# Performance work log

Hardware: AMD Instinct MI355X
Metric: run time of the kernel (lower is better)

Reference implementation:

```python
import jax, jax.numpy as jnp
import numpy as np

# Config (scaled-down DeepSeek-style MoE)
B, S, H = 4, 1024, 1024       # batch, seq, hidden_size
I = 512                        # intermediate_size per expert
E = 64                         # num_routed_experts
K = 8                          # top-k
C = 1024
NS = 1                         # num_shared_experts


def setup_inputs() -> dict:
    key = jax.random.key(0)
    ks = jax.random.split(key, 8)
    def w(k, shape, fan_in):
        return jax.random.normal(k, shape, jnp.float32) / np.float32(np.sqrt(fan_in))
    return {
        "hidden_states": jax.random.normal(ks[0], (B, S, H), jnp.float32),
        "gate_w":    w(ks[1], (E, H), H),            # nn.Linear(H, E).weight
        "shared_wg": w(ks[2], (I * NS, H), H),       # shared SwiGLU gate_proj
        "shared_wu": w(ks[3], (I * NS, H), H),       # shared SwiGLU up_proj
        "shared_wd": w(ks[4], (H, I * NS), I * NS),  # shared SwiGLU down_proj
        "expert_wg": w(ks[5], (E, I, H), H),         # routed gate_proj, stacked
        "expert_wu": w(ks[6], (E, I, H), H),         # routed up_proj, stacked
        "expert_wd": w(ks[7], (E, H, I), I),         # routed down_proj, stacked
    }


def reference(hidden_states, gate_w, shared_wg, shared_wu, shared_wd,
              expert_wg, expert_wu, expert_wd):
    b, s, h = hidden_states.shape
    x = hidden_states.reshape(-1, h)                     # [T, H]
    T = x.shape[0]

    # ---- shared expert (SwiGLU) ----
    shared = (jax.nn.silu(x @ shared_wg.T) * (x @ shared_wu.T)) @ shared_wd.T

    # ---- gating: sigmoid scores, top-k, normalize by sum ----
    scores = jax.nn.sigmoid(x @ gate_w.T)                # [T, E]
    topw, topi = jax.lax.top_k(scores, K)                # [T, K]
    topw = topw / topw.sum(-1, keepdims=True)

    # ---- dispatch: position of each (token, slot) within its expert ----
    e_flat = topi.reshape(-1)                            # [N] expert id per routed row
    N = e_flat.shape[0]
    order = jnp.argsort(e_flat)                          # rows sorted by expert id
    sorted_e = e_flat[order]
    seg_start = jnp.searchsorted(sorted_e, jnp.arange(E))
    pos_sorted = (jnp.arange(N) - seg_start[sorted_e]).astype(jnp.int32)
    pos = jnp.zeros(N, jnp.int32).at[order].set(pos_sorted)  # slot within expert buffer

    tok = jnp.repeat(jnp.arange(T), K)                   # token id per routed row
    xin = x[tok]                                         # [N, H]

    # scatter tokens into per-expert buffers [E, C, H]
    buf = jnp.zeros((E, C, h), x.dtype).at[e_flat, pos].set(xin, mode='drop')

    # per-expert SwiGLU via batched GEMMs (grouped-GEMM equivalent)
    g = jax.nn.silu(jnp.einsum('ech,eih->eci', buf, expert_wg))
    u = jnp.einsum('ech,eih->eci', buf, expert_wu)
    out_buf = jnp.einsum('eci,ehi->ech', g * u, expert_wd)  # [E, C, H]

    # gather back and combine with normalized top-k weights
    rows = out_buf[e_flat, pos]                          # [N, H]
    routed = (rows.reshape(T, K, h) * topw[..., None]).sum(1)

    return (shared + routed).reshape(b, s, h)
```

## Files before the change

kernel.cpp:

```cpp
#include <hip/hip_runtime.h>
#include <hip/hip_bf16.h>

#define TOK 4096
#define HD 1024
#define ID 512
#define NE 64
#define TK 8
#define CAP 1024
#define NROUTE 32768
#define NCHUNK 128

typedef __attribute__((ext_vector_type(4))) float f32x4;
typedef __attribute__((ext_vector_type(8))) short s16x8;
typedef __attribute__((ext_vector_type(2))) __bf16 bf16x2;

__device__ __forceinline__ ushort f2bf(float f){
  uint u = __builtin_bit_cast(uint, f);
  u += 0x7fffu + ((u >> 16) & 1u);
  return (ushort)(u >> 16);
}
__device__ __forceinline__ float bf2f(ushort b){
  uint u = ((uint)b) << 16;
  return __builtin_bit_cast(float, u);
}
__device__ __forceinline__ uint2 f4_to_bf4(float4 v){
  bf16x2 p0; p0[0] = (__bf16)v.x; p0[1] = (__bf16)v.y;
  bf16x2 p1; p1[0] = (__bf16)v.z; p1[1] = (__bf16)v.w;
  uint2 r; r.x = __builtin_bit_cast(uint, p0); r.y = __builtin_bit_cast(uint, p1);
  return r;
}
__device__ __forceinline__ short bfs(float f){
  __bf16 h = (__bf16)f;
  return __builtin_bit_cast(short, h);
}
__device__ __forceinline__ s16x8 pack8(float4 a, float4 b){
  s16x8 r;
  r[0]=bfs(a.x); r[1]=bfs(a.y); r[2]=bfs(a.z); r[3]=bfs(a.w);
  r[4]=bfs(b.x); r[5]=bfs(b.y); r[6]=bfs(b.z); r[7]=bfs(b.w);
  return r;
}
__device__ __forceinline__ void gld16(void* lds, const void* g){
  __builtin_amdgcn_global_load_lds((const __attribute__((address_space(1))) unsigned int*)g,
                                   (__attribute__((address_space(3))) unsigned int*)lds, 16, 0, 0);
}

__global__ __launch_bounds__(256)
void cvtX_kernel(const float* __restrict__ X, ushort* __restrict__ Xbf){
  size_t i = ((size_t)blockIdx.x*256 + threadIdx.x) * 8;
  float4 a = *(const float4*)(X + i);
  float4 b = *(const float4*)(X + i + 4);
  uint2 lo = f4_to_bf4(a), hi = f4_to_bf4(b);
  uint4 o; o.x = lo.x; o.y = lo.y; o.z = hi.x; o.w = hi.y;
  *(uint4*)(Xbf + i) = o;
}

__global__ __launch_bounds__(256)
void gating_kernel(const float* __restrict__ X, const float* __restrict__ GW,
                   int* __restrict__ topi, float* __restrict__ topw)
{
  __shared__ float xt[16][68];
  __shared__ float gt[64][68];
  __shared__ double ds[16][72];
  const int tid = threadIdx.x;
  const int tbase = blockIdx.x * 16;
  const int t = tid & 15, e0 = (tid >> 4) * 4;
  double acc[4] = {0.0, 0.0, 0.0, 0.0};
  for (int hc=0; hc<HD; hc+=64){
    { int r = tid >> 4, c4 = (tid & 15) * 4;
      *(float4*)&xt[r][c4] = *(const float4*)(X + (size_t)(tbase+r)*HD + hc + c4); }
    #pragma unroll
    for (int it=0; it<4; ++it){
      int idx = it*256 + tid;
      int r = idx >> 4, c4 = (idx & 15) * 4;
      *(float4*)&gt[r][c4] = *(const float4*)(GW + (size_t)r*HD + hc + c4);
    }
    __syncthreads();
    #pragma unroll
    for (int k4=0; k4<16; ++k4){
      float4 xv = *(const float4*)&xt[t][k4*4];
      #pragma unroll
      for (int j=0;j<4;++j){
        float4 gv = *(const float4*)&gt[e0+j][k4*4];
        acc[j] += (double)xv.x*(double)gv.x + (double)xv.y*(double)gv.y
                + (double)xv.z*(double)gv.z + (double)xv.w*(double)gv.w;
      }
    }
    __syncthreads();
  }
  #pragma unroll
  for (int j=0;j<4;++j) ds[t][e0+j] = acc[j];
  __syncthreads();
  if (tid < 16){
    int tt = tid;
    int idxs[8]; double vals[8]; double sum = 0.0;
    #pragma unroll
    for (int k=0;k<8;++k){
      double best = -1e300; int bi = 0;
      for (int e=0;e<NE;++e){ double v = ds[tt][e]; if (v > best){ best = v; bi = e; } }
      ds[tt][bi] = -1e300;
      double w = 1.0 / (1.0 + exp(-best));
      idxs[k] = bi; vals[k] = w; sum += w;
    }
    double inv = 1.0 / sum;
    #pragma unroll
    for (int k=0;k<8;++k){
      topi[(size_t)(tbase+tt)*TK + k] = idxs[k];
      topw[(size_t)(tbase+tt)*TK + k] = (float)(vals[k]*inv);
    }
  }
}

__global__ __launch_bounds__(256)
void hist_kernel(const int* __restrict__ topi, int* __restrict__ ccnt){
  __shared__ int h[NE];
  const int tid = threadIdx.x;
  if (tid < NE) h[tid] = 0;
  __syncthreads();
  atomicAdd(&h[topi[blockIdx.x*256 + tid]], 1);
  __syncthreads();
  if (tid < NE) ccnt[blockIdx.x*NE + tid] = h[tid];
}

__global__ __launch_bounds__(64)
void scan_kernel(const int* __restrict__ ccnt, int* __restrict__ cbase,
                 int* __restrict__ cntC, int* __restrict__ ebase){
  const int e = threadIdx.x;
  int run = 0;
  for (int c=0;c<NCHUNK;++c){ cbase[c*NE+e] = run; run += ccnt[c*NE+e]; }
  cntC[e] = run < CAP ? run : CAP;
  __syncthreads();
  if (e == 0){
    int s = 0;
    for (int i=0;i<NE;++i){ ebase[i] = s; s += cntC[i]; }
    ebase[NE] = s;
  }
}

__global__ __launch_bounds__(64)
void assign_kernel(const int* __restrict__ topi, const int* __restrict__ cbase,
                   int* __restrict__ pos, int* __restrict__ rowlist){
  __shared__ int es[256];
  const int tid = threadIdx.x;
  const int c = blockIdx.x;
  for (int i=tid;i<256;i+=64) es[i] = topi[c*256+i];
  __syncthreads();
  const int e = tid;
  int cntr = cbase[c*NE+e];
  for (int j=0;j<256;++j){
    if (es[j] == e){
      int n = c*256+j;
      pos[n] = cntr;
      if (cntr < CAP) rowlist[e*CAP + cntr] = n;
      ++cntr;
    }
  }
}

template<bool SHARED>
__global__ __launch_bounds__(256,2)
void gateup_kernel(const ushort* __restrict__ Xbf, const float* __restrict__ WG,
                   const float* __restrict__ WU, const int* __restrict__ rowlist,
                   const int* __restrict__ cntC, const int* __restrict__ ebase,
                   ushort* __restrict__ interm)
{
  int e, mt, nt, cnt, outbase;
  if (SHARED){
    nt = blockIdx.x & 7; mt = blockIdx.x >> 3; e = 0; cnt = TOK; outbase = mt*256;
  } else {
    int x = blockIdx.x & 7; int rem = blockIdx.x >> 3;
    nt = rem & 7; mt = (rem >> 3) & 3; e = ((rem >> 5) << 3) | x;
    cnt = cntC[e];
    if (mt*256 >= cnt) return;
    outbase = ebase[e] + mt*256;
  }
  const size_t wof = SHARED ? 0 : (size_t)e*ID*HD;
  const float* wg = WG + wof + (size_t)nt*64*HD;
  const float* wu = WU + wof + (size_t)nt*64*HD;

  __shared__ ushort aL[128*128];
  __shared__ ushort bL[64*128];
  __shared__ int tokb[256];

  const int tid = threadIdx.x;
  {
    int tokv;
    if (SHARED) tokv = mt*256 + tid;
    else tokv = (mt*256 + tid < cnt) ? (rowlist[e*CAP + mt*256 + tid] >> 3) : 0;
    tokb[tid] = tokv;
  }
  __syncthreads();

  const int w = tid >> 6, l = tid & 63;
  const int wm = w >> 1, wn = w & 1;
  const int fr = l & 15, fko = (l >> 4) * 8;

  uint aOff[8];
  #pragma unroll
  for (int j=0;j<8;++j){
    int f = j*256 + tid;
    int L = f >> 4, s = f & 15;
    int g = s ^ (L & 15);
    int r = 2*L + (g >> 3);
    aOff[j] = (uint)tokb[r]*HD + (uint)((g & 7)*8);
  }
  const float* bSrc[4]; int bDst[4];
  #pragma unroll
  for (int i=0;i<4;++i){
    int f = i*256 + tid;
    int L = f >> 4, s = f & 15;
    int g = s ^ (L & 15);
    int R = 2*L + (g >> 3);
    int gk = g & 7;
    bSrc[i] = ((R < 64) ? (wg + (size_t)R*HD) : (wu + (size_t)(R-64)*HD)) + gk*8;
    bDst[i] = f*8;
  }

  f32x4 acc[8][2][2];
  #pragma unroll
  for (int m=0;m<8;++m)
    #pragma unroll
    for (int a2=0;a2<2;++a2)
      #pragma unroll
      for (int c=0;c<2;++c) acc[m][a2][c] = (f32x4)0.0f;

  float4 br[4][2];

  auto loadB = [&](int kc){
    #pragma unroll
    for (int i=0;i<4;++i){
      br[i][0] = *(const float4*)(bSrc[i] + kc);
      br[i][1] = *(const float4*)(bSrc[i] + kc + 4);
    }
  };
  auto writeB = [&](){
    #pragma unroll
    for (int i=0;i<4;++i){
      *(s16x8*)&bL[bDst[i]] = pack8(br[i][0], br[i][1]);
    }
  };
  auto stageA = [&](int kc){
    #pragma unroll
    for (int j=0;j<8;++j) gld16(aL + (size_t)(j*256 + w*64)*8, Xbf + aOff[j] + kc);
  };

  loadB(0);
  stageA(0);
  for (int kc=0; kc<HD; kc+=64){
    __syncthreads();
    writeB();
    __syncthreads();
    s16x8 bfr[2][2][2];
    #pragma unroll
    for (int mat=0;mat<2;++mat)
      #pragma unroll
      for (int cg=0;cg<2;++cg)
        #pragma unroll
        for (int ks=0;ks<2;++ks){
          int R = mat*64 + wn*32 + cg*16 + fr;
          int gk = ks*4 + (fko>>3);
          int g = ((R&1)<<3) | gk;
          int L = R>>1;
          int gs = g ^ (L & 15);
          bfr[mat][cg][ks] = *(const s16x8*)&bL[L*128 + gs*8];
        }
    #pragma unroll
    for (int mb=0;mb<8;++mb){
      #pragma unroll
      for (int ks=0;ks<2;++ks){
        int r = wm*128 + mb*16 + fr;
        int gk = ks*4 + (fko>>3);
        int g = ((r&1)<<3) | gk;
        int L = r>>1;
        int gs = g ^ (L & 15);
        s16x8 a = *(const s16x8*)&aL[L*128 + gs*8];
        #pragma unroll
        for (int mat=0;mat<2;++mat)
          #pragma unroll
          for (int cg=0;cg<2;++cg)
            acc[mb][mat][cg] = __builtin_amdgcn_mfma_f32_16x16x32_bf16(a, bfr[mat][cg][ks], acc[mb][mat][cg], 0, 0, 0);
      }
    }
    __syncthreads();
    if (kc + 64 < HD){ loadB(kc + 64); stageA(kc + 64); }
  }

  const int rq = (l >> 4) * 4;
  #pragma unroll
  for (int mb=0;mb<8;++mb){
    #pragma unroll
    for (int q=0;q<4;++q){
      int rloc = wm*128 + mb*16 + rq + q;
      if (!SHARED && mt*256 + rloc >= cnt) continue;
      size_t orow = (size_t)(outbase + rloc);
      #pragma unroll
      for (int cg=0;cg<2;++cg){
        float g = acc[mb][0][cg][q], u = acc[mb][1][cg][q];
        float sv = g / (1.0f + __expf(-g)) * u;
        interm[orow*ID + (size_t)(nt*64 + wn*32 + cg*16 + fr)] = f2bf(sv);
      }
    }
  }
}

template<bool SHARED>
__global__ __launch_bounds__(256,2)
void down_kernel(const ushort* __restrict__ interm, const float* __restrict__ WD,
                 const int* __restrict__ cntC, const int* __restrict__ ebase,
                 ushort* __restrict__ out_rows, float* __restrict__ outf)
{
  int e, mt, nt, cnt, abase;
  if (SHARED){
    nt = blockIdx.x & 7; mt = blockIdx.x >> 3; e = 0; cnt = TOK; abase = mt*256;
  } else {
    int x = blockIdx.x & 7; int rem = blockIdx.x >> 3;
    nt = rem & 7; mt = (rem >> 3) & 3; e = ((rem >> 5) << 3) | x;
    cnt = cntC[e];
    if (mt*256 >= cnt) return;
    abase = ebase[e] + mt*256;
  }
  const ushort* A = interm + (size_t)abase*ID;
  const float* wd = WD + (SHARED ? (size_t)0 : (size_t)e*HD*ID) + (size_t)nt*128*ID;

  __shared__ ushort aL[128*128];
  __shared__ ushort bL[64*128];

  const int tid = threadIdx.x;
  const int w = tid >> 6, l = tid & 63;
  const int wm = w >> 1, wn = w & 1;
  const int fr = l & 15, fko = (l >> 4) * 8;

  uint aOff[8];
  #pragma unroll
  for (int j=0;j<8;++j){
    int f = j*256 + tid;
    int L = f >> 4, s = f & 15;
    int g = s ^ (L & 15);
    int r = 2*L + (g >> 3);
    aOff[j] = (uint)r*ID + (uint)((g & 7)*8);
  }
  const float* bSrc[4]; int bDst[4];
  #pragma unroll
  for (int i=0;i<4;++i){
    int f = i*256 + tid;
    int L = f >> 4, s = f & 15;
    int g = s ^ (L & 15);
    int R = 2*L + (g >> 3);
    int gk = g & 7;
    bSrc[i] = wd + (size_t)R*ID + gk*8;
    bDst[i] = f*8;
  }

  f32x4 acc[8][4];
  #pragma unroll
  for (int m=0;m<8;++m)
    #pragma unroll
    for (int c=0;c<4;++c) acc[m][c] = (f32x4)0.0f;

  float4 br[4][2];

  auto loadB = [&](int kc){
    #pragma unroll
    for (int i=0;i<4;++i){
      br[i][0] = *(const float4*)(bSrc[i] + kc);
      br[i][1] = *(const float4*)(bSrc[i] + kc + 4);
    }
  };
  auto writeB = [&](){
    #pragma unroll
    for (int i=0;i<4;++i){
      *(s16x8*)&bL[bDst[i]] = pack8(br[i][0], br[i][1]);
    }
  };
  auto stageA = [&](int kc){
    #pragma unroll
    for (int j=0;j<8;++j) gld16(aL + (size_t)(j*256 + w*64)*8, A + aOff[j] + kc);
  };

  loadB(0);
  stageA(0);
  for (int kc=0; kc<ID; kc+=64){
    __syncthreads();
    writeB();
    __syncthreads();
    s16x8 bfr[4][2];
    #pragma unroll
    for (int cg=0;cg<4;++cg)
      #pragma unroll
      for (int ks=0;ks<2;++ks){
        int R = wn*64 + cg*16 + fr;
        int gk = ks*4 + (fko>>3);
        int g = ((R&1)<<3) | gk;
        int L = R>>1;
        int gs = g ^ (L & 15);
        bfr[cg][ks] = *(const s16x8*)&bL[L*128 + gs*8];
      }
    #pragma unroll
    for (int mb=0;mb<8;++mb){
      #pragma unroll
      for (int ks=0;ks<2;++ks){
        int r = wm*128 + mb*16 + fr;
        int gk = ks*4 + (fko>>3);
        int g = ((r&1)<<3) | gk;
        int L = r>>1;
        int gs = g ^ (L & 15);
        s16x8 a = *(const s16x8*)&aL[L*128 + gs*8];
        #pragma unroll
        for (int cg=0;cg<4;++cg)
          acc[mb][cg] = __builtin_amdgcn_mfma_f32_16x16x32_bf16(a, bfr[cg][ks], acc[mb][cg], 0, 0, 0);
      }
    }
    __syncthreads();
    if (kc + 64 < ID){ loadB(kc + 64); stageA(kc + 64); }
  }

  const int rq = (l >> 4) * 4;
  #pragma unroll
  for (int mb=0;mb<8;++mb){
    #pragma unroll
    for (int q=0;q<4;++q){
      int rloc = wm*128 + mb*16 + rq + q;
      if (!SHARED && mt*256 + rloc >= cnt) continue;
      #pragma unroll
      for (int cg=0;cg<4;++cg){
        float v = acc[mb][cg][q];
        int colg = nt*128 + wn*64 + cg*16 + fr;
        if (SHARED) outf[(size_t)(mt*256 + rloc)*HD + colg] = v;
        else        out_rows[(size_t)(abase + rloc)*HD + colg] = f2bf(v);
      }
    }
  }
}

__global__ __launch_bounds__(256)
void combine_kernel(const int* __restrict__ topi, const float* __restrict__ topw,
                    const int* __restrict__ pos, const int* __restrict__ ebase,
                    const ushort* __restrict__ out_rows, float* __restrict__ out)
{
  const int t = blockIdx.x;
  const int tid = threadIdx.x;
  __shared__ int rws[TK];
  __shared__ float wts[TK];
  if (tid < TK){
    int e = topi[(size_t)t*TK + tid];
    int p = pos[(size_t)t*TK + tid];
    rws[tid] = (p < CAP) ? (ebase[e] + p) : -1;
    wts[tid] = topw[(size_t)t*TK + tid];
  }
  __syncthreads();
  const int h0 = tid * 4;
  float4 acc = *(float4*)(out + (size_t)t*HD + h0);
  #pragma unroll
  for (int k=0;k<TK;++k){
    int r = rws[k];
    if (r < 0) continue;
    ushort4 v = *(const ushort4*)(out_rows + (size_t)r*HD + h0);
    float wk = wts[k];
    acc.x += wk*bf2f(v.x); acc.y += wk*bf2f(v.y);
    acc.z += wk*bf2f(v.z); acc.w += wk*bf2f(v.w);
  }
  *(float4*)(out + (size_t)t*HD + h0) = acc;
}

extern "C" void kernel_launch(void* const* d_in, const int* in_sizes, int n_in,
                              void* d_out, int out_size, void* d_ws, size_t ws_size,
                              hipStream_t stream)
{
  (void)in_sizes; (void)n_in; (void)out_size; (void)ws_size;
  const float* X   = (const float*)d_in[0];
  const float* GW  = (const float*)d_in[1];
  const float* SWG = (const float*)d_in[2];
  const float* SWU = (const float*)d_in[3];
  const float* SWD = (const float*)d_in[4];
  const float* EWG = (const float*)d_in[5];
  const float* EWU = (const float*)d_in[6];
  const float* EWD = (const float*)d_in[7];
  float* OUT = (float*)d_out;

  char* p = (char*)d_ws;
  int*    topi    = (int*)p;      p += (size_t)NROUTE*4;
  float*  topw    = (float*)p;    p += (size_t)NROUTE*4;
  int*    pos     = (int*)p;      p += (size_t)NROUTE*4;
  int*    ccnt    = (int*)p;      p += (size_t)NCHUNK*NE*4;
  int*    cbase   = (int*)p;      p += (size_t)NCHUNK*NE*4;
  int*    cntC    = (int*)p;      p += 256;
  int*    ebase   = (int*)p;      p += 512;
  int*    rowlist = (int*)p;      p += (size_t)NE*CAP*4;
  ushort* Xbf     = (ushort*)p;   p += (size_t)TOK*HD*2;
  ushort* interm_r= (ushort*)p;   p += (size_t)(NROUTE+256)*ID*2;
  ushort* interm_s= (ushort*)p;   p += (size_t)TOK*ID*2;
  ushort* out_rows= (ushort*)p;   p += (size_t)NROUTE*HD*2;

  cvtX_kernel<<<TOK*HD/8/256, 256, 0, stream>>>(X, Xbf);
  gating_kernel<<<256, 256, 0, stream>>>(X, GW, topi, topw);
  hist_kernel<<<NCHUNK, 256, 0, stream>>>(topi, ccnt);
  scan_kernel<<<1, 64, 0, stream>>>(ccnt, cbase, cntC, ebase);
  assign_kernel<<<NCHUNK, 64, 0, stream>>>(topi, cbase, pos, rowlist);

  gateup_kernel<false><<<2048, 256, 0, stream>>>(Xbf, EWG, EWU, rowlist, cntC, ebase, interm_r);
  gateup_kernel<true ><<<128,  256, 0, stream>>>(Xbf, SWG, SWU, nullptr, nullptr, nullptr, interm_s);
  down_kernel<false><<<2048, 256, 0, stream>>>(interm_r, EWD, cntC, ebase, out_rows, nullptr);
  down_kernel<true ><<<128,  256, 0, stream>>>(interm_s, SWD, nullptr, nullptr, nullptr, OUT);

  combine_kernel<<<TOK, 256, 0, stream>>>(topi, topw, pos, ebase, out_rows, OUT);
}
```

Measured before the change: 399.9 us.

## Double-buffer LDS tiles and halve M tile in expert GEMMs

```diff
diff --git a/kernel.cpp b/kernel.cpp
--- a/kernel.cpp
+++ b/kernel.cpp
@@ -165,27 +165,27 @@
 {
   int e, mt, nt, cnt, outbase;
   if (SHARED){
-    nt = blockIdx.x & 7; mt = blockIdx.x >> 3; e = 0; cnt = TOK; outbase = mt*256;
+    nt = blockIdx.x & 7; mt = blockIdx.x >> 3; e = 0; cnt = TOK; outbase = mt*128;
   } else {
     int x = blockIdx.x & 7; int rem = blockIdx.x >> 3;
-    nt = rem & 7; mt = (rem >> 3) & 3; e = ((rem >> 5) << 3) | x;
+    nt = rem & 7; mt = (rem >> 3) & 7; e = ((rem >> 6) << 3) | x;
     cnt = cntC[e];
-    if (mt*256 >= cnt) return;
-    outbase = ebase[e] + mt*256;
+    if (mt*128 >= cnt) return;
+    outbase = ebase[e] + mt*128;
   }
   const size_t wof = SHARED ? 0 : (size_t)e*ID*HD;
   const float* wg = WG + wof + (size_t)nt*64*HD;
   const float* wu = WU + wof + (size_t)nt*64*HD;
 
-  __shared__ ushort aL[128*128];
-  __shared__ ushort bL[64*128];
-  __shared__ int tokb[256];
+  __shared__ ushort aL[2][64*128];
+  __shared__ ushort bL[2][64*128];
+  __shared__ int tokb[128];
 
   const int tid = threadIdx.x;
-  {
+  if (tid < 128){
     int tokv;
-    if (SHARED) tokv = mt*256 + tid;
-    else tokv = (mt*256 + tid < cnt) ? (rowlist[e*CAP + mt*256 + tid] >> 3) : 0;
+    if (SHARED) tokv = mt*128 + tid;
+    else tokv = (mt*128 + tid < cnt) ? (rowlist[e*CAP + mt*128 + tid] >> 3) : 0;
     tokb[tid] = tokv;
   }
   __syncthreads();
@@ -194,9 +194,9 @@
   const int wm = w >> 1, wn = w & 1;
   const int fr = l & 15, fko = (l >> 4) * 8;
 
-  uint aOff[8];
-  #pragma unroll
-  for (int j=0;j<8;++j){
+  uint aOff[4];
+  #pragma unroll
+  for (int j=0;j<4;++j){
     int f = j*256 + tid;
     int L = f >> 4, s = f & 15;
     int g = s ^ (L & 15);
@@ -215,9 +215,9 @@
     bDst[i] = f*8;
   }
 
-  f32x4 acc[8][2][2];
-  #pragma unroll
-  for (int m=0;m<8;++m)
+  f32x4 acc[4][2][2];
+  #pragma unroll
+  for (int m=0;m<4;++m)
     #pragma unroll
     for (int a2=0;a2<2;++a2)
       #pragma unroll
@@ -232,23 +232,22 @@
       br[i][1] = *(const float4*)(bSrc[i] + kc + 4);
     }
   };
-  auto writeB = [&](){
-    #pragma unroll
-    for (int i=0;i<4;++i){
-      *(s16x8*)&bL[bDst[i]] = pack8(br[i][0], br[i][1]);
-    }
+  auto writeB = [&](int b){
+    #pragma unroll
+    for (int i=0;i<4;++i) *(s16x8*)&bL[b][bDst[i]] = pack8(br[i][0], br[i][1]);
   };
-  auto stageA = [&](int kc){
-    #pragma unroll
-    for (int j=0;j<8;++j) gld16(aL + (size_t)(j*256 + w*64)*8, Xbf + aOff[j] + kc);
+  auto stageA = [&](int b, int kc){
+    #pragma unroll
+    for (int j=0;j<4;++j) gld16(&aL[b][(j*256 + w*64)*8], Xbf + aOff[j] + kc);
   };
 
-  loadB(0);
-  stageA(0);
-  for (int kc=0; kc<HD; kc+=64){
-    __syncthreads();
-    writeB();
-    __syncthreads();
+  loadB(0); stageA(0, 0); writeB(0);
+  __syncthreads();
+
+  for (int t=0; t<16; ++t){
+    const int cur = t & 1, nxt = cur ^ 1;
+    const int kc = t*64;
+    if (t < 15){ loadB(kc + 64); stageA(nxt, kc + 64); }
     s16x8 bfr[2][2][2];
     #pragma unroll
     for (int mat=0;mat<2;++mat)
@@ -261,18 +260,18 @@
           int g = ((R&1)<<3) | gk;
           int L = R>>1;
           int gs = g ^ (L & 15);
-          bfr[mat][cg][ks] = *(const s16x8*)&bL[L*128 + gs*8];
+          bfr[mat][cg][ks] = *(const s16x8*)&bL[cur][L*128 + gs*8];
         }
     #pragma unroll
-    for (int mb=0;mb<8;++mb){
+    for (int mb=0;mb<4;++mb){
       #pragma unroll
       for (int ks=0;ks<2;++ks){
-        int r = wm*128 + mb*16 + fr;
+        int r = wm*64 + mb*16 + fr;
         int gk = ks*4 + (fko>>3);
         int g = ((r&1)<<3) | gk;
         int L = r>>1;
         int gs = g ^ (L & 15);
-        s16x8 a = *(const s16x8*)&aL[L*128 + gs*8];
+        s16x8 a = *(const s16x8*)&aL[cur][L*128 + gs*8];
         #pragma unroll
         for (int mat=0;mat<2;++mat)
           #pragma unroll
@@ -280,17 +279,17 @@
             acc[mb][mat][cg] = __builtin_amdgcn_mfma_f32_16x16x32_bf16(a, bfr[mat][cg][ks], acc[mb][mat][cg], 0, 0, 0);
       }
     }
+    if (t < 15) writeB(nxt);
     __syncthreads();
-    if (kc + 64 < HD){ loadB(kc + 64); stageA(kc + 64); }
   }
 
   const int rq = (l >> 4) * 4;
   #pragma unroll
-  for (int mb=0;mb<8;++mb){
+  for (int mb=0;mb<4;++mb){
     #pragma unroll
     for (int q=0;q<4;++q){
-      int rloc = wm*128 + mb*16 + rq + q;
-      if (!SHARED && mt*256 + rloc >= cnt) continue;
+      int rloc = wm*64 + mb*16 + rq + q;
+      if (!SHARED && mt*128 + rloc >= cnt) continue;
       size_t orow = (size_t)(outbase + rloc);
       #pragma unroll
       for (int cg=0;cg<2;++cg){
@@ -310,28 +309,28 @@
 {
   int e, mt, nt, cnt, abase;
   if (SHARED){
-    nt = blockIdx.x & 7; mt = blockIdx.x >> 3; e = 0; cnt = TOK; abase = mt*256;
+    nt = blockIdx.x & 7; mt = blockIdx.x >> 3; e = 0; cnt = TOK; abase = mt*128;
   } else {
     int x = blockIdx.x & 7; int rem = blockIdx.x >> 3;
-    nt = rem & 7; mt = (rem >> 3) & 3; e = ((rem >> 5) << 3) | x;
+    nt = rem & 7; mt = (rem >> 3) & 7; e = ((rem >> 6) << 3) | x;
     cnt = cntC[e];
-    if (mt*256 >= cnt) return;
-    abase = ebase[e] + mt*256;
+    if (mt*128 >= cnt) return;
+    abase = ebase[e] + mt*128;
   }
   const ushort* A = interm + (size_t)abase*ID;
   const float* wd = WD + (SHARED ? (size_t)0 : (size_t)e*HD*ID) + (size_t)nt*128*ID;
 
-  __shared__ ushort aL[128*128];
-  __shared__ ushort bL[64*128];
+  __shared__ ushort aL[2][64*128];
+  __shared__ ushort bL[2][64*128];
 
   const int tid = threadIdx.x;
   const int w = tid >> 6, l = tid & 63;
   const int wm = w >> 1, wn = w & 1;
   const int fr = l & 15, fko = (l >> 4) * 8;
 
-  uint aOff[8];
-  #pragma unroll
-  for (int j=0;j<8;++j){
+  uint aOff[4];
+  #pragma unroll
+  for (int j=0;j<4;++j){
     int f = j*256 + tid;
     int L = f >> 4, s = f & 15;
     int g = s ^ (L & 15);
@@ -350,9 +349,9 @@
     bDst[i] = f*8;
   }
 
-  f32x4 acc[8][4];
-  #pragma unroll
-  for (int m=0;m<8;++m)
+  f32x4 acc[4][4];
+  #pragma unroll
+  for (int m=0;m<4;++m)
     #pragma unroll
     for (int c=0;c<4;++c) acc[m][c] = (f32x4)0.0f;
 
@@ -365,23 +364,22 @@
       br[i][1] = *(const float4*)(bSrc[i] + kc + 4);
     }
   };
-  auto writeB = [&](){
-    #pragma unroll
-    for (int i=0;i<4;++i){
-      *(s16x8*)&bL[bDst[i]] = pack8(br[i][0], br[i][1]);
-    }
+  auto writeB = [&](int b){
+    #pragma unroll
+    for (int i=0;i<4;++i) *(s16x8*)&bL[b][bDst[i]] = pack8(br[i][0], br[i][1]);
   };
-  auto stageA = [&](int kc){
-    #pragma unroll
-    for (int j=0;j<8;++j) gld16(aL + (size_t)(j*256 + w*64)*8, A + aOff[j] + kc);
+  auto stageA = [&](int b, int kc){
+    #pragma unroll
+    for (int j=0;j<4;++j) gld16(&aL[b][(j*256 + w*64)*8], A + aOff[j] + kc);
   };
 
-  loadB(0);
-  stageA(0);
-  for (int kc=0; kc<ID; kc+=64){
-    __syncthreads();
-    writeB();
-    __syncthreads();
+  loadB(0); stageA(0, 0); writeB(0);
+  __syncthreads();
+
+  for (int t=0; t<8; ++t){
+    const int cur = t & 1, nxt = cur ^ 1;
+    const int kc = t*64;
+    if (t < 7){ loadB(kc + 64); stageA(nxt, kc + 64); }
     s16x8 bfr[4][2];
     #pragma unroll
     for (int cg=0;cg<4;++cg)
@@ -392,39 +390,39 @@
         int g = ((R&1)<<3) | gk;
         int L = R>>1;
         int gs = g ^ (L & 15);
-        bfr[cg][ks] = *(const s16x8*)&bL[L*128 + gs*8];
+        bfr[cg][ks] = *(const s16x8*)&bL[cur][L*128 + gs*8];
       }
     #pragma unroll
-    for (int mb=0;mb<8;++mb){
+    for (int mb=0;mb<4;++mb){
       #pragma unroll
       for (int ks=0;ks<2;++ks){
-        int r = wm*128 + mb*16 + fr;
+        int r = wm*64 + mb*16 + fr;
         int gk = ks*4 + (fko>>3);
         int g = ((r&1)<<3) | gk;
         int L = r>>1;
         int gs = g ^ (L & 15);
-        s16x8 a = *(const s16x8*)&aL[L*128 + gs*8];
+        s16x8 a = *(const s16x8*)&aL[cur][L*128 + gs*8];
         #pragma unroll
         for (int cg=0;cg<4;++cg)
           acc[mb][cg] = __builtin_amdgcn_mfma_f32_16x16x32_bf16(a, bfr[cg][ks], acc[mb][cg], 0, 0, 0);
       }
     }
+    if (t < 7) writeB(nxt);
     __syncthreads();
-    if (kc + 64 < ID){ loadB(kc + 64); stageA(kc + 64); }
   }
 
   const int rq = (l >> 4) * 4;
   #pragma unroll
-  for (int mb=0;mb<8;++mb){
+  for (int mb=0;mb<4;++mb){
     #pragma unroll
     for (int q=0;q<4;++q){
-      int rloc = wm*128 + mb*16 + rq + q;
-      if (!SHARED && mt*256 + rloc >= cnt) continue;
+      int rloc = wm*64 + mb*16 + rq + q;
+      if (!SHARED && mt*128 + rloc >= cnt) continue;
       #pragma unroll
       for (int cg=0;cg<4;++cg){
         float v = acc[mb][cg][q];
         int colg = nt*128 + wn*64 + cg*16 + fr;
-        if (SHARED) outf[(size_t)(mt*256 + rloc)*HD + colg] = v;
+        if (SHARED) outf[(size_t)(mt*128 + rloc)*HD + colg] = v;
         else        out_rows[(size_t)(abase + rloc)*HD + colg] = f2bf(v);
       }
     }
@@ -496,10 +494,10 @@
   scan_kernel<<<1, 64, 0, stream>>>(ccnt, cbase, cntC, ebase);
   assign_kernel<<<NCHUNK, 64, 0, stream>>>(topi, cbase, pos, rowlist);
 
-  gateup_kernel<false><<<2048, 256, 0, stream>>>(Xbf, EWG, EWU, rowlist, cntC, ebase, interm_r);
-  gateup_kernel<true ><<<128,  256, 0, stream>>>(Xbf, SWG, SWU, nullptr, nullptr, nullptr, interm_s);
-  down_kernel<false><<<2048, 256, 0, stream>>>(interm_r, EWD, cntC, ebase, out_rows, nullptr);
-  down_kernel<true ><<<128,  256, 0, stream>>>(interm_s, SWD, nullptr, nullptr, nullptr, OUT);
+  gateup_kernel<false><<<4096, 256, 0, stream>>>(Xbf, EWG, EWU, rowlist, cntC, ebase, interm_r);
+  gateup_kernel<true ><<<256,  256, 0, stream>>>(Xbf, SWG, SWU, nullptr, nullptr, nullptr, interm_s);
+  down_kernel<false><<<4096, 256, 0, stream>>>(interm_r, EWD, cntC, ebase, out_rows, nullptr);
+  down_kernel<true ><<<256,  256, 0, stream>>>(interm_s, SWD, nullptr, nullptr, nullptr, OUT);
 
   combine_kernel<<<TOK, 256, 0, stream>>>(topi, topw, pos, ebase, out_rows, OUT);
 }
```

Result: slower. 443.2 us (+10.8%).

## Widen expert GEMM tiles to 8 waves and double-buffer LDS with deeper prefetch

Applied to the files above, without the earlier changes.

```diff
diff --git a/kernel.cpp b/kernel.cpp
--- a/kernel.cpp
+++ b/kernel.cpp
@@ -157,7 +157,7 @@
 }
 
 template<bool SHARED>
-__global__ __launch_bounds__(256,2)
+__global__ __launch_bounds__(512,1)
 void gateup_kernel(const ushort* __restrict__ Xbf, const float* __restrict__ WG,
                    const float* __restrict__ WU, const int* __restrict__ rowlist,
                    const int* __restrict__ cntC, const int* __restrict__ ebase,
@@ -165,24 +165,24 @@
 {
   int e, mt, nt, cnt, outbase;
   if (SHARED){
-    nt = blockIdx.x & 7; mt = blockIdx.x >> 3; e = 0; cnt = TOK; outbase = mt*256;
+    nt = blockIdx.x & 3; mt = blockIdx.x >> 2; e = 0; cnt = TOK; outbase = mt*256;
   } else {
     int x = blockIdx.x & 7; int rem = blockIdx.x >> 3;
-    nt = rem & 7; mt = (rem >> 3) & 3; e = ((rem >> 5) << 3) | x;
+    nt = rem & 3; mt = (rem >> 2) & 3; e = ((rem >> 4) << 3) | x;
     cnt = cntC[e];
     if (mt*256 >= cnt) return;
     outbase = ebase[e] + mt*256;
   }
   const size_t wof = SHARED ? 0 : (size_t)e*ID*HD;
-  const float* wg = WG + wof + (size_t)nt*64*HD;
-  const float* wu = WU + wof + (size_t)nt*64*HD;
-
-  __shared__ ushort aL[128*128];
-  __shared__ ushort bL[64*128];
+  const float* wg = WG + wof + (size_t)nt*128*HD;
+  const float* wu = WU + wof + (size_t)nt*128*HD;
+
+  __shared__ ushort aL[2][128*128];
+  __shared__ ushort bL[2][128*128];
   __shared__ int tokb[256];
 
   const int tid = threadIdx.x;
-  {
+  if (tid < 256){
     int tokv;
     if (SHARED) tokv = mt*256 + tid;
     else tokv = (mt*256 + tid < cnt) ? (rowlist[e*CAP + mt*256 + tid] >> 3) : 0;
@@ -191,98 +191,88 @@
   __syncthreads();
 
   const int w = tid >> 6, l = tid & 63;
-  const int wm = w >> 1, wn = w & 1;
+  const int wm = w >> 2, wn = w & 3;
   const int fr = l & 15, fko = (l >> 4) * 8;
 
-  uint aOff[8];
-  #pragma unroll
-  for (int j=0;j<8;++j){
-    int f = j*256 + tid;
+  uint aOff[4];
+  #pragma unroll
+  for (int j=0;j<4;++j){
+    int f = j*512 + tid;
     int L = f >> 4, s = f & 15;
     int g = s ^ (L & 15);
     int r = 2*L + (g >> 3);
     aOff[j] = (uint)tokb[r]*HD + (uint)((g & 7)*8);
   }
-  const float* bSrc[4]; int bDst[4];
+  const float* bsrc[4]; int bDst[4];
   #pragma unroll
   for (int i=0;i<4;++i){
-    int f = i*256 + tid;
+    int f = i*512 + tid;
     int L = f >> 4, s = f & 15;
     int g = s ^ (L & 15);
-    int R = 2*L + (g >> 3);
-    int gk = g & 7;
-    bSrc[i] = ((R < 64) ? (wg + (size_t)R*HD) : (wu + (size_t)(R-64)*HD)) + gk*8;
+    int b = 2*L + (g >> 3);
+    int n4 = b >> 6, r = b & 63;
+    int mat = r >> 5, c = r & 31;
+    const float* base = mat ? wu : wg;
+    bsrc[i] = base + (size_t)(n4*32 + c)*HD + (g & 7)*8;
     bDst[i] = f*8;
   }
 
-  f32x4 acc[8][2][2];
+  f32x4 accg[8][2], accu[8][2];
   #pragma unroll
   for (int m=0;m<8;++m)
     #pragma unroll
-    for (int a2=0;a2<2;++a2)
-      #pragma unroll
-      for (int c=0;c<2;++c) acc[m][a2][c] = (f32x4)0.0f;
-
-  float4 br[4][2];
-
-  auto loadB = [&](int kc){
-    #pragma unroll
-    for (int i=0;i<4;++i){
-      br[i][0] = *(const float4*)(bSrc[i] + kc);
-      br[i][1] = *(const float4*)(bSrc[i] + kc + 4);
-    }
-  };
-  auto writeB = [&](){
-    #pragma unroll
-    for (int i=0;i<4;++i){
-      *(s16x8*)&bL[bDst[i]] = pack8(br[i][0], br[i][1]);
-    }
-  };
-  auto stageA = [&](int kc){
-    #pragma unroll
-    for (int j=0;j<8;++j) gld16(aL + (size_t)(j*256 + w*64)*8, Xbf + aOff[j] + kc);
-  };
-
-  loadB(0);
-  stageA(0);
-  for (int kc=0; kc<HD; kc+=64){
-    __syncthreads();
-    writeB();
-    __syncthreads();
-    s16x8 bfr[2][2][2];
-    #pragma unroll
-    for (int mat=0;mat<2;++mat)
-      #pragma unroll
-      for (int cg=0;cg<2;++cg)
-        #pragma unroll
-        for (int ks=0;ks<2;++ks){
-          int R = mat*64 + wn*32 + cg*16 + fr;
-          int gk = ks*4 + (fko>>3);
-          int g = ((R&1)<<3) | gk;
-          int L = R>>1;
-          int gs = g ^ (L & 15);
-          bfr[mat][cg][ks] = *(const s16x8*)&bL[L*128 + gs*8];
-        }
-    #pragma unroll
-    for (int mb=0;mb<8;++mb){
-      #pragma unroll
-      for (int ks=0;ks<2;++ks){
-        int r = wm*128 + mb*16 + fr;
-        int gk = ks*4 + (fko>>3);
-        int g = ((r&1)<<3) | gk;
-        int L = r>>1;
-        int gs = g ^ (L & 15);
-        s16x8 a = *(const s16x8*)&aL[L*128 + gs*8];
-        #pragma unroll
-        for (int mat=0;mat<2;++mat)
-          #pragma unroll
-          for (int cg=0;cg<2;++cg)
-            acc[mb][mat][cg] = __builtin_amdgcn_mfma_f32_16x16x32_bf16(a, bfr[mat][cg][ks], acc[mb][mat][cg], 0, 0, 0);
-      }
-    }
-    __syncthreads();
-    if (kc + 64 < HD){ loadB(kc + 64); stageA(kc + 64); }
-  }
+    for (int c=0;c<2;++c){ accg[m][c] = (f32x4)0.0f; accu[m][c] = (f32x4)0.0f; }
+
+  float4 br0[8], br1[8];
+
+#define GU_LOADB(SET, kc) { _Pragma("unroll") for (int i=0;i<4;++i){ \
+    SET[2*i]   = *(const float4*)(bsrc[i] + (kc)); \
+    SET[2*i+1] = *(const float4*)(bsrc[i] + (kc) + 4); } }
+#define GU_WRITEB(BUF, SET) { _Pragma("unroll") for (int i=0;i<4;++i) \
+    *(s16x8*)&bL[BUF][bDst[i]] = pack8(SET[2*i], SET[2*i+1]); }
+#define GU_STAGEA(BUF, kc) { _Pragma("unroll") for (int j=0;j<4;++j) \
+    gld16(&aL[BUF][(j*512 + w*64)*8], Xbf + aOff[j] + (kc)); }
+#define GU_COMPUTE(BUF) { _Pragma("unroll") for (int ks=0;ks<2;++ks){ \
+    int gk = ks*4 + (fko>>3); \
+    s16x8 bg[2], bu[2]; \
+    _Pragma("unroll") for (int cg=0;cg<2;++cg){ \
+      int b1 = wn*64 + cg*16 + fr;      int L1 = b1>>1, g1 = ((b1&1)<<3)|gk; \
+      bg[cg] = *(const s16x8*)&bL[BUF][L1*128 + (g1^(L1&15))*8]; \
+      int b2 = wn*64 + 32 + cg*16 + fr; int L2 = b2>>1, g2 = ((b2&1)<<3)|gk; \
+      bu[cg] = *(const s16x8*)&bL[BUF][L2*128 + (g2^(L2&15))*8]; \
+    } \
+    _Pragma("unroll") for (int mb=0;mb<8;++mb){ \
+      int r = wm*128 + mb*16 + fr; \
+      int L = r>>1, g = ((r&1)<<3)|gk; \
+      s16x8 a = *(const s16x8*)&aL[BUF][L*128 + (g^(L&15))*8]; \
+      _Pragma("unroll") for (int cg=0;cg<2;++cg){ \
+        accg[mb][cg] = __builtin_amdgcn_mfma_f32_16x16x32_bf16(a, bg[cg], accg[mb][cg],0,0,0); \
+        accu[mb][cg] = __builtin_amdgcn_mfma_f32_16x16x32_bf16(a, bu[cg], accu[mb][cg],0,0,0); \
+      } } } }
+
+  GU_STAGEA(0, 0);
+  GU_LOADB(br0, 0);
+  GU_LOADB(br1, 64);
+  GU_WRITEB(0, br0);
+  __syncthreads();
+
+  for (int tt=0; tt<8; ++tt){
+    const int t0 = tt*2, t1 = tt*2+1;
+    if (t0 < 15) GU_STAGEA(1, (t0+1)*64);
+    if (t0 < 14) GU_LOADB(br0, (t0+2)*64);
+    if (t0 < 15) GU_WRITEB(1, br1);
+    GU_COMPUTE(0);
+    __syncthreads();
+    if (t1 < 15) GU_STAGEA(0, (t1+1)*64);
+    if (t1 < 14) GU_LOADB(br1, (t1+2)*64);
+    if (t1 < 15) GU_WRITEB(0, br0);
+    GU_COMPUTE(1);
+    __syncthreads();
+  }
+#undef GU_LOADB
+#undef GU_WRITEB
+#undef GU_STAGEA
+#undef GU_COMPUTE
 
   const int rq = (l >> 4) * 4;
   #pragma unroll
@@ -294,59 +284,58 @@
       size_t orow = (size_t)(outbase + rloc);
       #pragma unroll
       for (int cg=0;cg<2;++cg){
-        float g = acc[mb][0][cg][q], u = acc[mb][1][cg][q];
+        float g = accg[mb][cg][q], u = accu[mb][cg][q];
         float sv = g / (1.0f + __expf(-g)) * u;
-        interm[orow*ID + (size_t)(nt*64 + wn*32 + cg*16 + fr)] = f2bf(sv);
+        interm[orow*ID + (size_t)(nt*128 + wn*32 + cg*16 + fr)] = f2bf(sv);
       }
     }
   }
 }
 
 template<bool SHARED>
-__global__ __launch_bounds__(256,2)
+__global__ __launch_bounds__(512,1)
 void down_kernel(const ushort* __restrict__ interm, const float* __restrict__ WD,
                  const int* __restrict__ cntC, const int* __restrict__ ebase,
                  ushort* __restrict__ out_rows, float* __restrict__ outf)
 {
   int e, mt, nt, cnt, abase;
   if (SHARED){
-    nt = blockIdx.x & 7; mt = blockIdx.x >> 3; e = 0; cnt = TOK; abase = mt*256;
+    nt = blockIdx.x & 3; mt = blockIdx.x >> 2; e = 0; cnt = TOK; abase = mt*256;
   } else {
     int x = blockIdx.x & 7; int rem = blockIdx.x >> 3;
-    nt = rem & 7; mt = (rem >> 3) & 3; e = ((rem >> 5) << 3) | x;
+    nt = rem & 3; mt = (rem >> 2) & 3; e = ((rem >> 4) << 3) | x;
     cnt = cntC[e];
     if (mt*256 >= cnt) return;
     abase = ebase[e] + mt*256;
   }
   const ushort* A = interm + (size_t)abase*ID;
-  const float* wd = WD + (SHARED ? (size_t)0 : (size_t)e*HD*ID) + (size_t)nt*128*ID;
-
-  __shared__ ushort aL[128*128];
-  __shared__ ushort bL[64*128];
+  const float* wd = WD + (SHARED ? (size_t)0 : (size_t)e*HD*ID) + (size_t)nt*256*ID;
+
+  __shared__ ushort aL[2][128*128];
+  __shared__ ushort bL[2][128*128];
 
   const int tid = threadIdx.x;
   const int w = tid >> 6, l = tid & 63;
-  const int wm = w >> 1, wn = w & 1;
+  const int wm = w >> 2, wn = w & 3;
   const int fr = l & 15, fko = (l >> 4) * 8;
 
-  uint aOff[8];
-  #pragma unroll
-  for (int j=0;j<8;++j){
-    int f = j*256 + tid;
+  uint aOff[4];
+  #pragma unroll
+  for (int j=0;j<4;++j){
+    int f = j*512 + tid;
     int L = f >> 4, s = f & 15;
     int g = s ^ (L & 15);
     int r = 2*L + (g >> 3);
     aOff[j] = (uint)r*ID + (uint)((g & 7)*8);
   }
-  const float* bSrc[4]; int bDst[4];
+  const float* bsrc[4]; int bDst[4];
   #pragma unroll
   for (int i=0;i<4;++i){
-    int f = i*256 + tid;
+    int f = i*512 + tid;
     int L = f >> 4, s = f & 15;
     int g = s ^ (L & 15);
-    int R = 2*L + (g >> 3);
-    int gk = g & 7;
-    bSrc[i] = wd + (size_t)R*ID + gk*8;
+    int b = 2*L + (g >> 3);
+    bsrc[i] = wd + (size_t)b*ID + (g & 7)*8;
     bDst[i] = f*8;
   }
 
@@ -356,62 +345,53 @@
     #pragma unroll
     for (int c=0;c<4;++c) acc[m][c] = (f32x4)0.0f;
 
-  float4 br[4][2];
-
-  auto loadB = [&](int kc){
-    #pragma unroll
-    for (int i=0;i<4;++i){
-      br[i][0] = *(const float4*)(bSrc[i] + kc);
-      br[i][1] = *(const float4*)(bSrc[i] + kc + 4);
-    }
-  };
-  auto writeB = [&](){
-    #pragma unroll
-    for (int i=0;i<4;++i){
-      *(s16x8*)&bL[bDst[i]] = pack8(br[i][0], br[i][1]);
-    }
-  };
-  auto stageA = [&](int kc){
-    #pragma unroll
-    for (int j=0;j<8;++j) gld16(aL + (size_t)(j*256 + w*64)*8, A + aOff[j] + kc);
-  };
-
-  loadB(0);
-  stageA(0);
-  for (int kc=0; kc<ID; kc+=64){
-    __syncthreads();
-    writeB();
-    __syncthreads();
-    s16x8 bfr[4][2];
-    #pragma unroll
-    for (int cg=0;cg<4;++cg)
-      #pragma unroll
-      for (int ks=0;ks<2;++ks){
-        int R = wn*64 + cg*16 + fr;
-        int gk = ks*4 + (fko>>3);
-        int g = ((R&1)<<3) | gk;
-        int L = R>>1;
-        int gs = g ^ (L & 15);
-        bfr[cg][ks] = *(const s16x8*)&bL[L*128 + gs*8];
-      }
-    #pragma unroll
-    for (int mb=0;mb<8;++mb){
-      #pragma unroll
-      for (int ks=0;ks<2;++ks){
-        int r = wm*128 + mb*16 + fr;
-        int gk = ks*4 + (fko>>3);
-        int g = ((r&1)<<3) | gk;
-        int L = r>>1;
-        int gs = g ^ (L & 15);
-        s16x8 a = *(const s16x8*)&aL[L*128 + gs*8];
-        #pragma unroll
-        for (int cg=0;cg<4;++cg)
-          acc[mb][cg] = __builtin_amdgcn_mfma_f32_16x16x32_bf16(a, bfr[cg][ks], acc[mb][cg], 0, 0, 0);
-      }
-    }
-    __syncthreads();
-    if (kc + 64 < ID){ loadB(kc + 64); stageA(kc + 64); }
-  }
+  float4 br0[8], br1[8];
+
+#define DN_LOADB(SET, kc) { _Pragma("unroll") for (int i=0;i<4;++i){ \
+    SET[2*i]   = *(const float4*)(bsrc[i] + (kc)); \
+    SET[2*i+1] = *(const float4*)(bsrc[i] + (kc) + 4); } }
+#define DN_WRITEB(BUF, SET) { _Pragma("unroll") for (int i=0;i<4;++i) \
+    *(s16x8*)&bL[BUF][bDst[i]] = pack8(SET[2*i], SET[2*i+1]); }
+#define DN_STAGEA(BUF, kc) { _Pragma("unroll") for (int j=0;j<4;++j) \
+    gld16(&aL[BUF][(j*512 + w*64)*8], A + aOff[j] + (kc)); }
+#define DN_COMPUTE(BUF) { _Pragma("unroll") for (int ks=0;ks<2;++ks){ \
+    int gk = ks*4 + (fko>>3); \
+    s16x8 bd[4]; \
+    _Pragma("unroll") for (int cg=0;cg<4;++cg){ \
+      int b1 = wn*64 + cg*16 + fr; int L1 = b1>>1, g1 = ((b1&1)<<3)|gk; \
+      bd[cg] = *(const s16x8*)&bL[BUF][L1*128 + (g1^(L1&15))*8]; \
+    } \
+    _Pragma("unroll") for (int mb=0;mb<8;++mb){ \
+      int r = wm*128 + mb*16 + fr; \
+      int L = r>>1, g = ((r&1)<<3)|gk; \
+      s16x8 a = *(const s16x8*)&aL[BUF][L*128 + (g^(L&15))*8]; \
+      _Pragma("unroll") for (int cg=0;cg<4;++cg) \
+        acc[mb][cg] = __builtin_amdgcn_mfma_f32_16x16x32_bf16(a, bd[cg], acc[mb][cg],0,0,0); \
+    } } }
+
+  DN_STAGEA(0, 0);
+  DN_LOADB(br0, 0);
+  DN_LOADB(br1, 64);
+  DN_WRITEB(0, br0);
+  __syncthreads();
+
+  for (int tt=0; tt<4; ++tt){
+    const int t0 = tt*2, t1 = tt*2+1;
+    if (t0 < 7) DN_STAGEA(1, (t0+1)*64);
+    if (t0 < 6) DN_LOADB(br0, (t0+2)*64);
+    if (t0 < 7) DN_WRITEB(1, br1);
+    DN_COMPUTE(0);
+    __syncthreads();
+    if (t1 < 7) DN_STAGEA(0, (t1+1)*64);
+    if (t1 < 6) DN_LOADB(br1, (t1+2)*64);
+    if (t1 < 7) DN_WRITEB(0, br0);
+    DN_COMPUTE(1);
+    __syncthreads();
+  }
+#undef DN_LOADB
+#undef DN_WRITEB
+#undef DN_STAGEA
+#undef DN_COMPUTE
 
   const int rq = (l >> 4) * 4;
   #pragma unroll
@@ -423,7 +403,7 @@
       #pragma unroll
       for (int cg=0;cg<4;++cg){
         float v = acc[mb][cg][q];
-        int colg = nt*128 + wn*64 + cg*16 + fr;
+        int colg = nt*256 + wn*64 + cg*16 + fr;
         if (SHARED) outf[(size_t)(mt*256 + rloc)*HD + colg] = v;
         else        out_rows[(size_t)(abase + rloc)*HD + colg] = f2bf(v);
       }
@@ -496,10 +476,10 @@
   scan_kernel<<<1, 64, 0, stream>>>(ccnt, cbase, cntC, ebase);
   assign_kernel<<<NCHUNK, 64, 0, stream>>>(topi, cbase, pos, rowlist);
 
-  gateup_kernel<false><<<2048, 256, 0, stream>>>(Xbf, EWG, EWU, rowlist, cntC, ebase, interm_r);
-  gateup_kernel<true ><<<128,  256, 0, stream>>>(Xbf, SWG, SWU, nullptr, nullptr, nullptr, interm_s);
-  down_kernel<false><<<2048, 256, 0, stream>>>(interm_r, EWD, cntC, ebase, out_rows, nullptr);
-  down_kernel<true ><<<128,  256, 0, stream>>>(interm_s, SWD, nullptr, nullptr, nullptr, OUT);
+  gateup_kernel<false><<<1024, 512, 0, stream>>>(Xbf, EWG, EWU, rowlist, cntC, ebase, interm_r);
+  gateup_kernel<true ><<<64,   512, 0, stream>>>(Xbf, SWG, SWU, nullptr, nullptr, nullptr, interm_s);
+  down_kernel<false><<<1024, 512, 0, stream>>>(interm_r, EWD, cntC, ebase, out_rows, nullptr);
+  down_kernel<true ><<<64,   512, 0, stream>>>(interm_s, SWD, nullptr, nullptr, nullptr, OUT);
 
   combine_kernel<<<TOK, 256, 0, stream>>>(topi, topw, pos, ebase, out_rows, OUT);
 }
```

After: 597.5 us. 1.49x slower.

## Double-buffer A tiles in LDS and load B fragments directly from global

Applied to the files above, without the earlier changes.

```diff
diff --git a/kernel.cpp b/kernel.cpp
--- a/kernel.cpp
+++ b/kernel.cpp
@@ -177,8 +177,7 @@
   const float* wg = WG + wof + (size_t)nt*64*HD;
   const float* wu = WU + wof + (size_t)nt*64*HD;
 
-  __shared__ ushort aL[128*128];
-  __shared__ ushort bL[64*128];
+  __shared__ ushort aL[2][128*128];
   __shared__ int tokb[256];
 
   const int tid = threadIdx.x;
@@ -203,85 +202,68 @@
     int r = 2*L + (g >> 3);
     aOff[j] = (uint)tokb[r]*HD + (uint)((g & 7)*8);
   }
-  const float* bSrc[4]; int bDst[4];
-  #pragma unroll
-  for (int i=0;i<4;++i){
-    int f = i*256 + tid;
-    int L = f >> 4, s = f & 15;
-    int g = s ^ (L & 15);
-    int R = 2*L + (g >> 3);
-    int gk = g & 7;
-    bSrc[i] = ((R < 64) ? (wg + (size_t)R*HD) : (wu + (size_t)(R-64)*HD)) + gk*8;
-    bDst[i] = f*8;
-  }
-
-  f32x4 acc[8][2][2];
+  const float* bp[2][2];
+  #pragma unroll
+  for (int mat=0;mat<2;++mat)
+    #pragma unroll
+    for (int cg=0;cg<2;++cg){
+      int R = wn*32 + cg*16 + fr;
+      bp[mat][cg] = (mat ? wu : wg) + (size_t)R*HD + fko;
+    }
+
+  f32x4 accg[8][2], accu[8][2];
   #pragma unroll
   for (int m=0;m<8;++m)
     #pragma unroll
-    for (int a2=0;a2<2;++a2)
-      #pragma unroll
-      for (int c=0;c<2;++c) acc[m][a2][c] = (f32x4)0.0f;
-
-  float4 br[4][2];
-
-  auto loadB = [&](int kc){
-    #pragma unroll
-    for (int i=0;i<4;++i){
-      br[i][0] = *(const float4*)(bSrc[i] + kc);
-      br[i][1] = *(const float4*)(bSrc[i] + kc + 4);
-    }
+    for (int c=0;c<2;++c){ accg[m][c] = (f32x4)0.0f; accu[m][c] = (f32x4)0.0f; }
+
+  auto stageA = [&](int b, int kc){
+    #pragma unroll
+    for (int j=0;j<8;++j) gld16(&aL[b][(j*256 + w*64)*8], Xbf + aOff[j] + kc);
   };
-  auto writeB = [&](){
-    #pragma unroll
-    for (int i=0;i<4;++i){
-      *(s16x8*)&bL[bDst[i]] = pack8(br[i][0], br[i][1]);
-    }
-  };
-  auto stageA = [&](int kc){
-    #pragma unroll
-    for (int j=0;j<8;++j) gld16(aL + (size_t)(j*256 + w*64)*8, Xbf + aOff[j] + kc);
-  };
-
-  loadB(0);
-  stageA(0);
-  for (int kc=0; kc<HD; kc+=64){
-    __syncthreads();
-    writeB();
-    __syncthreads();
-    s16x8 bfr[2][2][2];
+  auto compute = [&](int b, int kc){
+    float4 bv[2][2][2][2];
     #pragma unroll
     for (int mat=0;mat<2;++mat)
       #pragma unroll
       for (int cg=0;cg<2;++cg)
         #pragma unroll
         for (int ks=0;ks<2;++ks){
-          int R = mat*64 + wn*32 + cg*16 + fr;
-          int gk = ks*4 + (fko>>3);
-          int g = ((R&1)<<3) | gk;
-          int L = R>>1;
-          int gs = g ^ (L & 15);
-          bfr[mat][cg][ks] = *(const s16x8*)&bL[L*128 + gs*8];
+          bv[mat][cg][ks][0] = *(const float4*)(bp[mat][cg] + kc + ks*32);
+          bv[mat][cg][ks][1] = *(const float4*)(bp[mat][cg] + kc + ks*32 + 4);
         }
-    #pragma unroll
-    for (int mb=0;mb<8;++mb){
-      #pragma unroll
-      for (int ks=0;ks<2;++ks){
+    s16x8 bfr[2][2][2];
+    #pragma unroll
+    for (int mat=0;mat<2;++mat)
+      #pragma unroll
+      for (int cg=0;cg<2;++cg)
+        #pragma unroll
+        for (int ks=0;ks<2;++ks)
+          bfr[mat][cg][ks] = pack8(bv[mat][cg][ks][0], bv[mat][cg][ks][1]);
+    #pragma unroll
+    for (int ks=0;ks<2;++ks){
+      int gk = ks*4 + (fko>>3);
+      #pragma unroll
+      for (int mb=0;mb<8;++mb){
         int r = wm*128 + mb*16 + fr;
-        int gk = ks*4 + (fko>>3);
-        int g = ((r&1)<<3) | gk;
-        int L = r>>1;
-        int gs = g ^ (L & 15);
-        s16x8 a = *(const s16x8*)&aL[L*128 + gs*8];
+        int L = r>>1, g = ((r&1)<<3)|gk;
+        s16x8 a = *(const s16x8*)&aL[b][L*128 + (g^(L&15))*8];
         #pragma unroll
-        for (int mat=0;mat<2;++mat)
-          #pragma unroll
-          for (int cg=0;cg<2;++cg)
-            acc[mb][mat][cg] = __builtin_amdgcn_mfma_f32_16x16x32_bf16(a, bfr[mat][cg][ks], acc[mb][mat][cg], 0, 0, 0);
-      }
-    }
+        for (int cg=0;cg<2;++cg){
+          accg[mb][cg] = __builtin_amdgcn_mfma_f32_16x16x32_bf16(a, bfr[0][cg][ks], accg[mb][cg],0,0,0);
+          accu[mb][cg] = __builtin_amdgcn_mfma_f32_16x16x32_bf16(a, bfr[1][cg][ks], accu[mb][cg],0,0,0);
+        }
+      }
+    }
+  };
+
+  stageA(0, 0);
+  __syncthreads();
+  for (int t=0; t<16; ++t){
+    const int cur = t & 1;
+    if (t < 15) stageA(cur ^ 1, (t+1)*64);
+    compute(cur, t*64);
     __syncthreads();
-    if (kc + 64 < HD){ loadB(kc + 64); stageA(kc + 64); }
   }
 
   const int rq = (l >> 4) * 4;
@@ -294,7 +276,7 @@
       size_t orow = (size_t)(outbase + rloc);
       #pragma unroll
       for (int cg=0;cg<2;++cg){
-        float g = acc[mb][0][cg][q], u = acc[mb][1][cg][q];
+        float g = accg[mb][cg][q], u = accu[mb][cg][q];
         float sv = g / (1.0f + __expf(-g)) * u;
         interm[orow*ID + (size_t)(nt*64 + wn*32 + cg*16 + fr)] = f2bf(sv);
       }
@@ -321,8 +303,8 @@
   const ushort* A = interm + (size_t)abase*ID;
   const float* wd = WD + (SHARED ? (size_t)0 : (size_t)e*HD*ID) + (size_t)nt*128*ID;
 
-  __shared__ ushort aL[128*128];
-  __shared__ ushort bL[64*128];
+  __shared__ ushort aL[2][64*128];
+  __shared__ ushort aL2[2][64*128];
 
   const int tid = threadIdx.x;
   const int w = tid >> 6, l = tid & 63;
@@ -338,16 +320,11 @@
     int r = 2*L + (g >> 3);
     aOff[j] = (uint)r*ID + (uint)((g & 7)*8);
   }
-  const float* bSrc[4]; int bDst[4];
-  #pragma unroll
-  for (int i=0;i<4;++i){
-    int f = i*256 + tid;
-    int L = f >> 4, s = f & 15;
-    int g = s ^ (L & 15);
-    int R = 2*L + (g >> 3);
-    int gk = g & 7;
-    bSrc[i] = wd + (size_t)R*ID + gk*8;
-    bDst[i] = f*8;
+  const float* bp[4];
+  #pragma unroll
+  for (int cg=0;cg<4;++cg){
+    int R = wn*64 + cg*16 + fr;
+    bp[cg] = wd + (size_t)R*ID + fko;
   }
 
   f32x4 acc[8][4];
@@ -356,61 +333,51 @@
     #pragma unroll
     for (int c=0;c<4;++c) acc[m][c] = (f32x4)0.0f;
 
-  float4 br[4][2];
-
-  auto loadB = [&](int kc){
-    #pragma unroll
-    for (int i=0;i<4;++i){
-      br[i][0] = *(const float4*)(bSrc[i] + kc);
-      br[i][1] = *(const float4*)(bSrc[i] + kc + 4);
-    }
+  auto ldsAt = [&](int b, int off)->ushort* {
+    return (off < 64*128) ? &aL[b][off] : &aL2[b][off - 64*128];
   };
-  auto writeB = [&](){
-    #pragma unroll
-    for (int i=0;i<4;++i){
-      *(s16x8*)&bL[bDst[i]] = pack8(br[i][0], br[i][1]);
-    }
+  auto stageA = [&](int b, int kc){
+    #pragma unroll
+    for (int j=0;j<8;++j) gld16(ldsAt(b, (j*256 + w*64)*8), A + aOff[j] + kc);
   };
-  auto stageA = [&](int kc){
-    #pragma unroll
-    for (int j=0;j<8;++j) gld16(aL + (size_t)(j*256 + w*64)*8, A + aOff[j] + kc);
-  };
-
-  loadB(0);
-  stageA(0);
-  for (int kc=0; kc<ID; kc+=64){
-    __syncthreads();
-    writeB();
-    __syncthreads();
+  auto compute = [&](int b, int kc){
+    float4 bv[4][2][2];
+    #pragma unroll
+    for (int cg=0;cg<4;++cg)
+      #pragma unroll
+      for (int ks=0;ks<2;++ks){
+        bv[cg][ks][0] = *(const float4*)(bp[cg] + kc + ks*32);
+        bv[cg][ks][1] = *(const float4*)(bp[cg] + kc + ks*32 + 4);
+      }
     s16x8 bfr[4][2];
     #pragma unroll
     for (int cg=0;cg<4;++cg)
       #pragma unroll
-      for (int ks=0;ks<2;++ks){
-        int R = wn*64 + cg*16 + fr;
-        int gk = ks*4 + (fko>>3);
-        int g = ((R&1)<<3) | gk;
-        int L = R>>1;
-        int gs = g ^ (L & 15);
-        bfr[cg][ks] = *(const s16x8*)&bL[L*128 + gs*8];
-      }
-    #pragma unroll
-    for (int mb=0;mb<8;++mb){
-      #pragma unroll
-      for (int ks=0;ks<2;++ks){
+      for (int ks=0;ks<2;++ks)
+        bfr[cg][ks] = pack8(bv[cg][ks][0], bv[cg][ks][1]);
+    #pragma unroll
+    for (int ks=0;ks<2;++ks){
+      int gk = ks*4 + (fko>>3);
+      #pragma unroll
+      for (int mb=0;mb<8;++mb){
         int r = wm*128 + mb*16 + fr;
-        int gk = ks*4 + (fko>>3);
-        int g = ((r&1)<<3) | gk;
-        int L = r>>1;
-        int gs = g ^ (L & 15);
-        s16x8 a = *(const s16x8*)&aL[L*128 + gs*8];
+        int L = r>>1, g = ((r&1)<<3)|gk;
+        int off = L*128 + (g^(L&15))*8;
+        s16x8 a = *(const s16x8*)ldsAt(b, off);
         #pragma unroll
         for (int cg=0;cg<4;++cg)
-          acc[mb][cg] = __builtin_amdgcn_mfma_f32_16x16x32_bf16(a, bfr[cg][ks], acc[mb][cg], 0, 0, 0);
-      }
-    }
+          acc[mb][cg] = __builtin_amdgcn_mfma_f32_16x16x32_bf16(a, bfr[cg][ks], acc[mb][cg],0,0,0);
+      }
+    }
+  };
+
+  stageA(0, 0);
+  __syncthreads();
+  for (int t=0; t<8; ++t){
+    const int cur = t & 1;
+    if (t < 7) stageA(cur ^ 1, (t+1)*64);
+    compute(cur, t*64);
     __syncthreads();
-    if (kc + 64 < ID){ loadB(kc + 64); stageA(kc + 64); }
   }
 
   const int rq = (l >> 4) * 4;
```

New measurement: 609.0 us. 1.52x slower.
